# Performance work log

Hardware: AMD Instinct MI355X
Metric: run time of the kernel (lower is better)

The kernel has to match this reference:

```python
import jax, jax.numpy as jnp
import numpy as np

B, S, HID, NH, DH = 2, 1024, 4096, 32, 128
ACT_BITS, W_BITS = 8, 4
NEG_INF = float(np.finfo(np.float32).min)


def _qdq(x, bits):
    """Symmetric fake-quant over the last axis (per-token / per-out-channel), with STE."""
    qmax = 2.0 ** (bits - 1) - 1
    s = jnp.maximum(jnp.max(jnp.abs(x), axis=-1, keepdims=True) / qmax, 1e-8)
    q = jnp.clip(jnp.round(x / s), -qmax - 1, qmax) * s
    return x + jax.lax.stop_gradient(q - x)


def _rope_tables(seq_len, dim):
    inv_freq = 1.0 / (10000.0 ** (np.arange(0, dim, 2, dtype=np.float32) / dim))
    t = np.arange(seq_len, dtype=np.float32)
    freqs = np.outer(t, inv_freq)              # [S, DH/2]
    emb = np.concatenate([freqs, freqs], -1)   # [S, DH]
    return jnp.asarray(np.cos(emb)), jnp.asarray(np.sin(emb))


def _rotate_half(x):
    h = x.shape[-1] // 2
    return jnp.concatenate([-x[..., h:], x[..., :h]], axis=-1)


def _norm(x):
    return jnp.linalg.norm(x, axis=-1, keepdims=True)


def setup_inputs() -> dict:
    key = jax.random.key(0)
    ks = jax.random.split(key, 5)
    causal = jnp.where(jnp.tril(jnp.ones((S, S), dtype=bool)), 0.0, NEG_INF).astype(jnp.float32)
    return {
        "hidden_states": jax.random.normal(ks[0], (B, S, HID), jnp.float32),
        "wq": jax.random.normal(ks[1], (HID, HID), jnp.float32) * 0.02,
        "wk": jax.random.normal(ks[2], (HID, HID), jnp.float32) * 0.02,
        "wv": jax.random.normal(ks[3], (HID, HID), jnp.float32) * 0.02,
        "wo": jax.random.normal(ks[4], (HID, HID), jnp.float32) * 0.02,
        "attention_mask": jnp.broadcast_to(causal[None, None], (B, 1, S, S)),
    }


def reference(hidden_states, wq, wk, wv, wo, attention_mask):
    cos, sin = _rope_tables(S, DH)
    cos, sin = cos[None, None], sin[None, None]          # [1,1,S,DH]
    x = _qdq(hidden_states, ACT_BITS)                    # act fake-quant (per token)

    def proj(w):
        return jnp.einsum('bsh,dh->bsd', x, _qdq(w, W_BITS)).reshape(B, S, NH, DH).transpose(0, 2, 1, 3)

    q, k, v = proj(wq), proj(wk), proj(wv)               # [B,H,S,D]
    q = q * cos + _rotate_half(q) * sin
    k = k * cos + _rotate_half(k) * sin

    # qkt_matmul: quant Q and K, rescale scores by quantization norm ratios a1, a2
    x1len = _norm(q)
    qq = _qdq(q, ACT_BITS)
    a1 = _norm(qq) / x1len                               # [B,H,S,1]
    x2len = _norm(k)
    kq = _qdq(k, ACT_BITS)
    a2 = jnp.swapaxes(_norm(kq) / x2len, 2, 3)           # [B,H,1,S]

    attn = jnp.einsum('bhqd,bhkd->bhqk', qq, kq) / np.float32(np.sqrt(DH))
    attn = attn / a1 / a2
    attn = attn + attention_mask
    attn = jnp.maximum(attn, NEG_INF)
    p = jax.nn.softmax(attn.astype(jnp.float32), axis=-1)

    # pv_matmul: quant P and V, rescale output by V's norm ratio
    pq = _qdq(p, ACT_BITS)
    x2len_v = _norm(v)
    vq = _qdq(v, ACT_BITS)
    a2v = _norm(vq) / x2len_v                            # [B,H,S,1]

    out = jnp.einsum('bhqk,bhkd->bhqd', pq, vq) / a2v    # [B,H,S,D]
    out = out.transpose(0, 2, 1, 3).reshape(B, S, HID)
    out = jnp.einsum('bsh,dh->bsd', _qdq(out, ACT_BITS), _qdq(wo, W_BITS))
    return out
```

## Files before the change

kernel.cpp:

```cpp
#include <hip/hip_runtime.h>
#include <hip/hip_bf16.h>
#include <math.h>
#include <stdint.h>

#define NEG_INF_F (-3.4028234663852886e38f)

typedef __bf16 bf16_t;
typedef __bf16 bf16x8 __attribute__((ext_vector_type(8)));
typedef float f32x4 __attribute__((ext_vector_type(4)));
typedef float f32x16 __attribute__((ext_vector_type(16)));
typedef int i32x4 __attribute__((ext_vector_type(4)));
typedef int i32x16 __attribute__((ext_vector_type(16)));
typedef int8_t c8x4 __attribute__((ext_vector_type(4)));

static constexpr int Bb = 2, Ss = 1024, Hid = 4096, Nh = 32, Dh = 128;
static constexpr int Mr = Bb * Ss;
static constexpr int Bh = Bb * Nh;

__device__ __forceinline__ void gload_lds16(const void* g, void* l) {
  __builtin_amdgcn_global_load_lds((const __attribute__((address_space(1))) void*)g,
                                   (__attribute__((address_space(3))) void*)l, 16, 0, 0);
}

__device__ __forceinline__ float wred_max(float v) {
#pragma unroll
  for (int off = 32; off > 0; off >>= 1) v = fmaxf(v, __shfl_xor(v, off));
  return v;
}

__device__ __forceinline__ unsigned pkbf(float a, float b) {
  unsigned short ua = __builtin_bit_cast(unsigned short, (bf16_t)a);
  unsigned short ub = __builtin_bit_cast(unsigned short, (bf16_t)b);
  return (unsigned)ua | ((unsigned)ub << 16);
}

__global__ void rope_table_kernel(float* __restrict__ ctab, float* __restrict__ stab) {
  int i = blockIdx.x * 256 + threadIdx.x;
  int srow = i >> 6, d = i & 63;
  float invf = (float)pow(10000.0, -((double)(2 * d) / (double)Dh));
  float ang = (float)srow * invf;
  ctab[i] = (float)cos((double)ang);
  stab[i] = (float)sin((double)ang);
}

__global__ __launch_bounds__(256) void quant_rows_kernel(
    const float* __restrict__ in, int8_t* __restrict__ outq,
    float* __restrict__ scale, int ncols, float qmax, float clo, float chi)
{
  const int row = blockIdx.x;
  const float* x = in + (size_t)row * ncols;
  int8_t* o = outq + (size_t)row * ncols;
  const int tid = threadIdx.x;
  const float4* x4 = (const float4*)x;
  const int n4 = ncols >> 2;
  float m = 0.f;
  for (int i = tid; i < n4; i += 256) {
    float4 v = x4[i];
    m = fmaxf(m, fmaxf(fmaxf(fabsf(v.x), fabsf(v.y)), fmaxf(fabsf(v.z), fabsf(v.w))));
  }
  m = wred_max(m);
  __shared__ float red[4];
  if ((tid & 63) == 0) red[tid >> 6] = m;
  __syncthreads();
  m = fmaxf(fmaxf(red[0], red[1]), fmaxf(red[2], red[3]));
  const float s = fmaxf(m / qmax, 1e-8f);
  if (tid == 0) scale[row] = s;
  c8x4* o4 = (c8x4*)o;
  for (int i = tid; i < n4; i += 256) {
    float4 v = x4[i];
    c8x4 r;
    r[0] = (int8_t)(int)fminf(fmaxf(rintf(v.x / s), clo), chi);
    r[1] = (int8_t)(int)fminf(fmaxf(rintf(v.y / s), clo), chi);
    r[2] = (int8_t)(int)fminf(fmaxf(rintf(v.z / s), clo), chi);
    r[3] = (int8_t)(int)fminf(fmaxf(rintf(v.w / s), clo), chi);
    o4[i] = r;
  }
}

__global__ __launch_bounds__(256) void gemm_kernel(
    const int8_t* __restrict__ A, const float* __restrict__ sA,
    const int8_t* __restrict__ W, const float* __restrict__ sW,
    float* __restrict__ out, int M, int N, int K, int mode)
{
  __shared__ __align__(16) int8_t As[128 * 64];
  __shared__ __align__(16) int8_t Bs[128 * 64];
  const int tid = threadIdx.x, lane = tid & 63, wid = tid >> 6;
  const int bm = blockIdx.x * 128, bn = blockIdx.y * 128;
  const int wm = wid >> 1, wn = wid & 1;
  const int l15 = lane & 15, kg = lane >> 4;

  const int srow = wid * 16 + (lane >> 2);
  const int skin = (lane & 3) * 16;
  const int8_t* gA = A + (size_t)(bm + srow) * K + skin;
  const int8_t* gB = W + (size_t)(bn + srow) * K + skin;
  const size_t half = (size_t)64 * K;
  int8_t* lA = As + wid * 1024;
  int8_t* lB = Bs + wid * 1024;

  i32x4 acc[4][4] = {};
  for (int k0 = 0; k0 < K; k0 += 64) {
    if (k0) __syncthreads();
    gload_lds16(gA + k0, lA);
    gload_lds16(gA + k0 + half, lA + 4096);
    gload_lds16(gB + k0, lB);
    gload_lds16(gB + k0 + half, lB + 4096);
    __syncthreads();
    i32x4 af[4], bw[4];
#pragma unroll
    for (int f = 0; f < 4; ++f) {
      af[f] = *(const i32x4*)&As[(wm * 64 + f * 16 + l15) * 64 + kg * 16];
      bw[f] = *(const i32x4*)&Bs[(wn * 64 + f * 16 + l15) * 64 + kg * 16];
    }
#pragma unroll
    for (int fm = 0; fm < 4; ++fm)
#pragma unroll
      for (int fn = 0; fn < 4; ++fn)
        acc[fm][fn] = __builtin_amdgcn_mfma_i32_16x16x64_i8(af[fm], bw[fn], acc[fm][fn], 0, 0, 0);
  }
#pragma unroll
  for (int fm = 0; fm < 4; ++fm) {
    const int row0 = bm + wm * 64 + fm * 16 + kg * 4;
#pragma unroll
    for (int fn = 0; fn < 4; ++fn) {
      const int col = bn + wn * 64 + fn * 16 + l15;
      const float swv = sW[col];
#pragma unroll
      for (int j = 0; j < 4; ++j) {
        const int row = row0 + j;
        const float val = (float)acc[fm][fn][j] * sA[row] * swv;
        size_t off;
        if (mode == 0) off = (size_t)row * N + col;
        else {
          int b = row >> 10, si = row & 1023, h = col >> 7, d = col & 127;
          off = (((size_t)(b * Nh + h)) * Ss + si) * Dh + d;
        }
        out[off] = val;
      }
    }
  }
}

__global__ __launch_bounds__(256) void rope_quant_kernel(
    const float* __restrict__ xin,
    const float* __restrict__ ctab, const float* __restrict__ stab,
    int8_t* __restrict__ xq, float* __restrict__ F)
{
  const int gid = blockIdx.x * 4 + (threadIdx.x >> 6);
  const int lane = threadIdx.x & 63;
  const int srow = gid & (Ss - 1);
  const float* x = xin + (size_t)gid * Dh;
  const float xl = x[lane], xh = x[lane + 64];
  const float c = ctab[srow * 64 + lane], sn = stab[srow * 64 + lane];
  const float rl = __fsub_rn(__fmul_rn(xl, c), __fmul_rn(xh, sn));
  const float rh = __fadd_rn(__fmul_rn(xh, c), __fmul_rn(xl, sn));
  float ma = fmaxf(fabsf(rl), fabsf(rh));
  float n2 = rl * rl + rh * rh;
#pragma unroll
  for (int off = 32; off > 0; off >>= 1) {
    ma = fmaxf(ma, __shfl_xor(ma, off));
    n2 += __shfl_xor(n2, off);
  }
  const float s = fmaxf(ma / 127.0f, 1e-8f);
  const float ql = fminf(fmaxf(rintf(rl / s), -128.f), 127.f);
  const float qh = fminf(fmaxf(rintf(rh / s), -128.f), 127.f);
  float nq2 = ql * ql + qh * qh;
#pragma unroll
  for (int off = 32; off > 0; off >>= 1) nq2 += __shfl_xor(nq2, off);
  int8_t* o = xq + (size_t)gid * Dh;
  o[lane] = (int8_t)(int)ql;
  o[lane + 64] = (int8_t)(int)qh;
  if (lane == 0) F[gid] = sqrtf(n2 / nq2) * 0.2973017787506803f;
}

__global__ __launch_bounds__(256) void vquant_kernel(
    const float* __restrict__ vin, bf16_t* __restrict__ vdqt, float* __restrict__ a2v)
{
  __shared__ bf16_t s_v[128 * 66];
  const int tid = threadIdx.x, lane = tid & 63;
  const int l15 = lane & 15;
  const int qw = (tid >> 6) * 4 + (lane >> 4);
  const int bh = blockIdx.x >> 4;
  const int t0 = (blockIdx.x & 15) * 64;
  for (int it = 0; it < 4; ++it) {
    const int tt = qw * 4 + it;
    const size_t gid = (size_t)bh * Ss + t0 + tt;
    const float4 va = *(const float4*)(vin + gid * Dh + l15 * 8);
    const float4 vb = *(const float4*)(vin + gid * Dh + l15 * 8 + 4);
    float m = fmaxf(fmaxf(fmaxf(fabsf(va.x), fabsf(va.y)), fmaxf(fabsf(va.z), fabsf(va.w))),
                    fmaxf(fmaxf(fabsf(vb.x), fabsf(vb.y)), fmaxf(fabsf(vb.z), fabsf(vb.w))));
    float n2 = va.x * va.x + va.y * va.y + va.z * va.z + va.w * va.w +
               vb.x * vb.x + vb.y * vb.y + vb.z * vb.z + vb.w * vb.w;
#pragma unroll
    for (int off = 1; off < 16; off <<= 1) {
      m = fmaxf(m, __shfl_xor(m, off));
      n2 += __shfl_xor(n2, off);
    }
    const float s = fmaxf(m / 127.0f, 1e-8f);
    float q[8] = {va.x, va.y, va.z, va.w, vb.x, vb.y, vb.z, vb.w};
    float nq2 = 0.f;
#pragma unroll
    for (int e = 0; e < 8; ++e) {
      q[e] = fminf(fmaxf(rintf(q[e] / s), -128.f), 127.f);
      nq2 += q[e] * q[e];
      s_v[(l15 * 8 + e) * 66 + tt] = (bf16_t)(q[e] * s);
    }
#pragma unroll
    for (int off = 1; off < 16; off <<= 1) nq2 += __shfl_xor(nq2, off);
    if (l15 == 0) a2v[gid] = s * sqrtf(nq2) / sqrtf(n2);
  }
  __syncthreads();
  const int r = tid >> 1, hc = (tid & 1) * 32;
  const bf16_t* src = &s_v[r * 66 + hc];
  bf16_t* dst = vdqt + ((size_t)bh * Dh + r) * Ss + t0 + hc;
#pragma unroll
  for (int k = 0; k < 4; ++k) {
    bf16x8 t;
#pragma unroll
    for (int e = 0; e < 8; ++e) t[e] = src[k * 8 + e];
    *(bf16x8*)(dst + k * 8) = t;
  }
}

#define KR(r) (((r) & 3) + 8 * ((r) >> 2) + 4 * hi)
__global__ __launch_bounds__(64, 2) void attn_kernel(
    const int8_t* __restrict__ qq, const int8_t* __restrict__ kq,
    const bf16_t* __restrict__ vdqt,
    const float* __restrict__ Fq, const float* __restrict__ Fk,
    const float* __restrict__ A2v, float* __restrict__ oattn)
{
  const int bh = blockIdx.x, b = bh >> 5, h = bh & 31;
  const int lane = threadIdx.x & 63;
  const int l31 = lane & 31, hi = lane >> 5;
  const int u = 31 - (int)blockIdx.y;
  const int q0 = u * 32;
  const int nt = u + 1;
  const size_t bhS = (size_t)bh * Ss;

  const int8_t* qrow = qq + (bhS + q0 + l31) * Dh + hi * 16;
  i32x4 qf[4];
#pragma unroll
  for (int c = 0; c < 4; ++c) qf[c] = *(const i32x4*)(qrow + c * 32);
  const float fq = Fq[bhS + q0 + l31];
  const int qcol = q0 + l31;

  float m = NEG_INF_F;
  int t = 0;
  for (; t + 1 < nt; t += 2) {
    const int kb0 = t * 32, kb1 = kb0 + 32;
    const int8_t* kr0 = kq + (bhS + kb0 + l31) * Dh + hi * 16;
    const int8_t* kr1 = kq + (bhS + kb1 + l31) * Dh + hi * 16;
    i32x16 ca = {}, cb = {}, da = {}, db = {};
    ca = __builtin_amdgcn_mfma_i32_32x32x32_i8(*(const i32x4*)(kr0),      qf[0], ca, 0, 0, 0);
    cb = __builtin_amdgcn_mfma_i32_32x32x32_i8(*(const i32x4*)(kr0 + 64), qf[2], cb, 0, 0, 0);
    da = __builtin_amdgcn_mfma_i32_32x32x32_i8(*(const i32x4*)(kr1),      qf[0], da, 0, 0, 0);
    db = __builtin_amdgcn_mfma_i32_32x32x32_i8(*(const i32x4*)(kr1 + 64), qf[2], db, 0, 0, 0);
    ca = __builtin_amdgcn_mfma_i32_32x32x32_i8(*(const i32x4*)(kr0 + 32), qf[1], ca, 0, 0, 0);
    cb = __builtin_amdgcn_mfma_i32_32x32x32_i8(*(const i32x4*)(kr0 + 96), qf[3], cb, 0, 0, 0);
    da = __builtin_amdgcn_mfma_i32_32x32x32_i8(*(const i32x4*)(kr1 + 32), qf[1], da, 0, 0, 0);
    db = __builtin_amdgcn_mfma_i32_32x32x32_i8(*(const i32x4*)(kr1 + 96), qf[3], db, 0, 0, 0);
    float4 fk40[4], fk41[4];
#pragma unroll
    for (int g = 0; g < 4; ++g) fk40[g] = *(const float4*)&Fk[bhS + kb0 + g * 8 + 4 * hi];
#pragma unroll
    for (int g = 0; g < 4; ++g) fk41[g] = *(const float4*)&Fk[bhS + kb1 + g * 8 + 4 * hi];
    const bool diag1 = (t + 1 == nt - 1);
#pragma unroll
    for (int r = 0; r < 16; ++r) {
      m = fmaxf(m, (float)(ca[r] + cb[r]) * fq * ((const float*)&fk40[r >> 2])[r & 3]);
      const float v1 = (float)(da[r] + db[r]) * fq * ((const float*)&fk41[r >> 2])[r & 3];
      if (!diag1 || (kb1 + KR(r) <= qcol)) m = fmaxf(m, v1);
    }
  }
  if (t < nt) {
    const int kb = t * 32;
    const int8_t* krow = kq + (bhS + kb + l31) * Dh + hi * 16;
    i32x16 ca = {}, cb = {};
    ca = __builtin_amdgcn_mfma_i32_32x32x32_i8(*(const i32x4*)(krow),      qf[0], ca, 0, 0, 0);
    cb = __builtin_amdgcn_mfma_i32_32x32x32_i8(*(const i32x4*)(krow + 64), qf[2], cb, 0, 0, 0);
    ca = __builtin_amdgcn_mfma_i32_32x32x32_i8(*(const i32x4*)(krow + 32), qf[1], ca, 0, 0, 0);
    cb = __builtin_amdgcn_mfma_i32_32x32x32_i8(*(const i32x4*)(krow + 96), qf[3], cb, 0, 0, 0);
    float4 fk4[4];
#pragma unroll
    for (int g = 0; g < 4; ++g) fk4[g] = *(const float4*)&Fk[bhS + kb + g * 8 + 4 * hi];
#pragma unroll
    for (int r = 0; r < 16; ++r) {
      const float v = (float)(ca[r] + cb[r]) * fq * ((const float*)&fk4[r >> 2])[r & 3];
      if (kb + KR(r) <= qcol) m = fmaxf(m, v);
    }
  }
  m = fmaxf(m, __shfl_xor(m, 32));

  float z = 0.f;
  f32x16 oacc[4] = {};
  for (int tt = 0; tt < nt; ++tt) {
    const int kb = tt * 32;
    const int8_t* krow = kq + (bhS + kb + l31) * Dh + hi * 16;
    i32x16 ca = {}, cb = {};
    ca = __builtin_amdgcn_mfma_i32_32x32x32_i8(*(const i32x4*)(krow),      qf[0], ca, 0, 0, 0);
    cb = __builtin_amdgcn_mfma_i32_32x32x32_i8(*(const i32x4*)(krow + 64), qf[2], cb, 0, 0, 0);
    ca = __builtin_amdgcn_mfma_i32_32x32x32_i8(*(const i32x4*)(krow + 32), qf[1], ca, 0, 0, 0);
    cb = __builtin_amdgcn_mfma_i32_32x32x32_i8(*(const i32x4*)(krow + 96), qf[3], cb, 0, 0, 0);
    float4 fk4[4];
#pragma unroll
    for (int g = 0; g < 4; ++g) fk4[g] = *(const float4*)&Fk[bhS + kb + g * 8 + 4 * hi];
    float p[16];
    const bool diag = (tt == nt - 1);
#pragma unroll
    for (int r = 0; r < 16; ++r) {
      float v = (float)(ca[r] + cb[r]) * fq * ((const float*)&fk4[r >> 2])[r & 3];
      if (diag && (kb + KR(r) > qcol)) v = NEG_INF_F;
      const float e = __expf(v - m);
      z += e;
      p[r] = rintf(127.0f * e);
    }
#pragma unroll
    for (int s = 0; s < 2; ++s) {
      const int rs = s * 8;
      unsigned k0 = pkbf(p[rs + 0], p[rs + 1]);
      unsigned k1 = pkbf(p[rs + 2], p[rs + 3]);
      unsigned k2 = pkbf(p[rs + 4], p[rs + 5]);
      unsigned k3 = pkbf(p[rs + 6], p[rs + 7]);
      unsigned sx0 = __shfl_xor(k0, 32);
      unsigned sx1 = __shfl_xor(k1, 32);
      unsigned sx2 = __shfl_xor(k2, 32);
      unsigned sx3 = __shfl_xor(k3, 32);
      uint4 ww;
      ww.x = hi ? sx2 : k0;
      ww.y = hi ? sx3 : k1;
      ww.z = hi ? k2 : sx0;
      ww.w = hi ? k3 : sx1;
      const bf16x8 af = __builtin_bit_cast(bf16x8, ww);
      const int kg = kb + s * 16 + hi * 8;
#pragma unroll
      for (int dt = 0; dt < 4; ++dt) {
        const bf16x8 vf = *(const bf16x8*)(vdqt + ((size_t)bh * Dh + dt * 32 + l31) * Ss + kg);
        oacc[dt] = __builtin_amdgcn_mfma_f32_32x32x16_bf16(af, vf, oacc[dt], 0, 0, 0);
      }
    }
  }
  z += __shfl_xor(z, 32);
  const float osc = (1.0f / z) / 127.0f / A2v[bhS + q0 + l31];
#pragma unroll
  for (int dt = 0; dt < 4; ++dt) {
#pragma unroll
    for (int r = 0; r < 16; ++r) {
      const int q = q0 + KR(r);
      const float oscr = __shfl(osc, KR(r));
      oattn[((size_t)b * Ss + q) * Hid + h * Dh + dt * 32 + l31] = oacc[dt][r] * oscr;
    }
  }
}

extern "C" void kernel_launch(void* const* d_in, const int* in_sizes, int n_in,
                              void* d_out, int out_size, void* d_ws, size_t ws_size,
                              hipStream_t stream)
{
  const float* hidden = (const float*)d_in[0];
  const float* wq = (const float*)d_in[1];
  const float* wk = (const float*)d_in[2];
  const float* wv = (const float*)d_in[3];
  const float* wo = (const float*)d_in[4];
  float* out = (float*)d_out;

  char* p = (char*)d_ws;
  auto alloc = [&](size_t bytes) -> char* {
    char* r = p; p += (bytes + 255) & ~(size_t)255; return r;
  };
  int8_t* xq   = (int8_t*)alloc((size_t)Mr * Hid);
  int8_t* wbuf = (int8_t*)alloc((size_t)Hid * Hid);
  float*  projf= (float*) alloc((size_t)Bh * Ss * Dh * sizeof(float));
  int8_t* qqb  = (int8_t*)alloc((size_t)Bh * Ss * Dh);
  int8_t* kqb  = (int8_t*)alloc((size_t)Bh * Ss * Dh);
  bf16_t* vdqt = (bf16_t*)alloc((size_t)Bh * Dh * Ss * sizeof(bf16_t));
  float* sxa = (float*)alloc((size_t)Mr * sizeof(float));
  float* sw  = (float*)alloc((size_t)Hid * sizeof(float));
  float* Fq  = (float*)alloc((size_t)Bh * Ss * sizeof(float));
  float* Fk  = (float*)alloc((size_t)Bh * Ss * sizeof(float));
  float* A2v = (float*)alloc((size_t)Bh * Ss * sizeof(float));
  float* soa = (float*)alloc((size_t)Mr * sizeof(float));
  float* ctab = (float*)alloc((size_t)Ss * 64 * sizeof(float));
  float* stab = (float*)alloc((size_t)Ss * 64 * sizeof(float));
  float*  oat = projf;
  int8_t* oq  = xq;

  rope_table_kernel<<<Ss * 64 / 256, 256, 0, stream>>>(ctab, stab);
  quant_rows_kernel<<<Mr, 256, 0, stream>>>(hidden, xq, sxa, Hid, 127.f, -128.f, 127.f);

  dim3 gg(Mr / 128, Hid / 128);
  quant_rows_kernel<<<Hid, 256, 0, stream>>>(wq, wbuf, sw, Hid, 7.f, -8.f, 7.f);
  gemm_kernel<<<gg, 256, 0, stream>>>(xq, sxa, wbuf, sw, projf, Mr, Hid, Hid, 1);
  rope_quant_kernel<<<Bh * Ss / 4, 256, 0, stream>>>(projf, ctab, stab, qqb, Fq);
  quant_rows_kernel<<<Hid, 256, 0, stream>>>(wk, wbuf, sw, Hid, 7.f, -8.f, 7.f);
  gemm_kernel<<<gg, 256, 0, stream>>>(xq, sxa, wbuf, sw, projf, Mr, Hid, Hid, 1);
  rope_quant_kernel<<<Bh * Ss / 4, 256, 0, stream>>>(projf, ctab, stab, kqb, Fk);
  quant_rows_kernel<<<Hid, 256, 0, stream>>>(wv, wbuf, sw, Hid, 7.f, -8.f, 7.f);
  gemm_kernel<<<gg, 256, 0, stream>>>(xq, sxa, wbuf, sw, projf, Mr, Hid, Hid, 1);
  vquant_kernel<<<Bh * 16, 256, 0, stream>>>(projf, vdqt, A2v);

  dim3 ga(Bh, 32);
  attn_kernel<<<ga, 64, 0, stream>>>(qqb, kqb, vdqt, Fq, Fk, A2v, oat);

  quant_rows_kernel<<<Mr, 256, 0, stream>>>(oat, oq, soa, Hid, 127.f, -128.f, 127.f);
  quant_rows_kernel<<<Hid, 256, 0, stream>>>(wo, wbuf, sw, Hid, 7.f, -8.f, 7.f);
  gemm_kernel<<<gg, 256, 0, stream>>>(oq, soa, wbuf, sw, out, Mr, Hid, Hid, 0);
}
```

Measured before the change: 446.9 us.

## Fuse RoPE and per-head quantization into QKV GEMM epilogues, swizzle LDS and blocks

Q/K projection GEMMs now apply RoPE, per-token-per-head int8 quantization and the norm-ratio factor directly in the epilogue. The V GEMM quantizes, transposes through shared memory and writes bf16 V^T plus A2v. This removes the fp32 projection round-trip and the separate rope_quant and vquant kernels. Column fragments are remapped so each 128-wide N tile holds one head with matching rotate-half pairs in registers. The change also adds an XOR swizzle on the LDS k-chunks and an XCD-aware block ordering, at the cost of more registers and extra epilogue syncs.

```diff
diff --git a/kernel.cpp b/kernel.cpp
--- a/kernel.cpp
+++ b/kernel.cpp
@@ -77,22 +77,36 @@
   }
 }
 
+template <int MODE>
 __global__ __launch_bounds__(256) void gemm_kernel(
     const int8_t* __restrict__ A, const float* __restrict__ sA,
     const int8_t* __restrict__ W, const float* __restrict__ sW,
-    float* __restrict__ out, int M, int N, int K, int mode)
+    float* __restrict__ out0,
+    int8_t* __restrict__ outq, float* __restrict__ Ff,
+    bf16_t* __restrict__ vdq, float* __restrict__ a2vp,
+    const float* __restrict__ ctab, const float* __restrict__ stab,
+    int M, int N, int K)
 {
   __shared__ __align__(16) int8_t As[128 * 64];
   __shared__ __align__(16) int8_t Bs[128 * 64];
+  __shared__ float s_red[2][128][3];
+  __shared__ __align__(16) char smem_vt[MODE == 3 ? (128 * 136 * 2) : 16];
+
   const int tid = threadIdx.x, lane = tid & 63, wid = tid >> 6;
-  const int bm = blockIdx.x * 128, bn = blockIdx.y * 128;
+  const int id = blockIdx.x;
+  const int xcd = id & 7, within = id >> 3;
+  const int nIdx = xcd * 4 + (within >> 4);
+  const int mIdx = within & 15;
+  const int bm = mIdx * 128, bn = nIdx * 128;
+
   const int wm = wid >> 1, wn = wid & 1;
   const int l15 = lane & 15, kg = lane >> 4;
-
-  const int srow = wid * 16 + (lane >> 2);
-  const int skin = (lane & 3) * 16;
-  const int8_t* gA = A + (size_t)(bm + srow) * K + skin;
-  const int8_t* gB = W + (size_t)(bn + srow) * K + skin;
+  const int ckey = (l15 >> 1) & 3;
+
+  const int srowL = wid * 16 + (lane >> 2);
+  const int skin = ((lane & 3) ^ ((lane >> 3) & 3)) * 16;
+  const int8_t* gA = A + (size_t)(bm + srowL) * K + skin;
+  const int8_t* gB = W + (size_t)(bn + srowL) * K + skin;
   const size_t half = (size_t)64 * K;
   int8_t* lA = As + wid * 1024;
   int8_t* lB = Bs + wid * 1024;
@@ -108,8 +122,8 @@
     i32x4 af[4], bw[4];
 #pragma unroll
     for (int f = 0; f < 4; ++f) {
-      af[f] = *(const i32x4*)&As[(wm * 64 + f * 16 + l15) * 64 + kg * 16];
-      bw[f] = *(const i32x4*)&Bs[(wn * 64 + f * 16 + l15) * 64 + kg * 16];
+      af[f] = *(const i32x4*)&As[(wm * 64 + f * 16 + l15) * 64 + (kg ^ ckey) * 16];
+      bw[f] = *(const i32x4*)&Bs[(f * 32 + wn * 16 + l15) * 64 + (kg ^ ckey) * 16];
     }
 #pragma unroll
     for (int fm = 0; fm < 4; ++fm)
@@ -117,107 +131,169 @@
       for (int fn = 0; fn < 4; ++fn)
         acc[fm][fn] = __builtin_amdgcn_mfma_i32_16x16x64_i8(af[fm], bw[fn], acc[fm][fn], 0, 0, 0);
   }
-#pragma unroll
-  for (int fm = 0; fm < 4; ++fm) {
-    const int row0 = bm + wm * 64 + fm * 16 + kg * 4;
-#pragma unroll
-    for (int fn = 0; fn < 4; ++fn) {
-      const int col = bn + wn * 64 + fn * 16 + l15;
-      const float swv = sW[col];
+
+  float sav[4][4], swv[4];
+#pragma unroll
+  for (int fm = 0; fm < 4; ++fm)
+#pragma unroll
+    for (int j = 0; j < 4; ++j) sav[fm][j] = sA[bm + wm * 64 + fm * 16 + kg * 4 + j];
+#pragma unroll
+  for (int fn = 0; fn < 4; ++fn) swv[fn] = sW[bn + fn * 32 + wn * 16 + l15];
+
+  float val[4][4][4];
+#pragma unroll
+  for (int fm = 0; fm < 4; ++fm)
+#pragma unroll
+    for (int fn = 0; fn < 4; ++fn)
+#pragma unroll
+      for (int j = 0; j < 4; ++j)
+        val[fm][fn][j] = (float)acc[fm][fn][j] * sav[fm][j] * swv[fn];
+
+  if constexpr (MODE == 0) {
+#pragma unroll
+    for (int fm = 0; fm < 4; ++fm)
 #pragma unroll
       for (int j = 0; j < 4; ++j) {
-        const int row = row0 + j;
-        const float val = (float)acc[fm][fn][j] * sA[row] * swv;
-        size_t off;
-        if (mode == 0) off = (size_t)row * N + col;
-        else {
-          int b = row >> 10, si = row & 1023, h = col >> 7, d = col & 127;
-          off = (((size_t)(b * Nh + h)) * Ss + si) * Dh + d;
-        }
-        out[off] = val;
+        const int row = bm + wm * 64 + fm * 16 + kg * 4 + j;
+#pragma unroll
+        for (int fn = 0; fn < 4; ++fn)
+          out0[(size_t)row * N + bn + fn * 32 + wn * 16 + l15] = val[fm][fn][j];
       }
-    }
-  }
-}
-
-__global__ __launch_bounds__(256) void rope_quant_kernel(
-    const float* __restrict__ xin,
-    const float* __restrict__ ctab, const float* __restrict__ stab,
-    int8_t* __restrict__ xq, float* __restrict__ F)
-{
-  const int gid = blockIdx.x * 4 + (threadIdx.x >> 6);
-  const int lane = threadIdx.x & 63;
-  const int srow = gid & (Ss - 1);
-  const float* x = xin + (size_t)gid * Dh;
-  const float xl = x[lane], xh = x[lane + 64];
-  const float c = ctab[srow * 64 + lane], sn = stab[srow * 64 + lane];
-  const float rl = __fsub_rn(__fmul_rn(xl, c), __fmul_rn(xh, sn));
-  const float rh = __fadd_rn(__fmul_rn(xh, c), __fmul_rn(xl, sn));
-  float ma = fmaxf(fabsf(rl), fabsf(rh));
-  float n2 = rl * rl + rh * rh;
-#pragma unroll
-  for (int off = 32; off > 0; off >>= 1) {
-    ma = fmaxf(ma, __shfl_xor(ma, off));
-    n2 += __shfl_xor(n2, off);
-  }
-  const float s = fmaxf(ma / 127.0f, 1e-8f);
-  const float ql = fminf(fmaxf(rintf(rl / s), -128.f), 127.f);
-  const float qh = fminf(fmaxf(rintf(rh / s), -128.f), 127.f);
-  float nq2 = ql * ql + qh * qh;
-#pragma unroll
-  for (int off = 32; off > 0; off >>= 1) nq2 += __shfl_xor(nq2, off);
-  int8_t* o = xq + (size_t)gid * Dh;
-  o[lane] = (int8_t)(int)ql;
-  o[lane + 64] = (int8_t)(int)qh;
-  if (lane == 0) F[gid] = sqrtf(n2 / nq2) * 0.2973017787506803f;
-}
-
-__global__ __launch_bounds__(256) void vquant_kernel(
-    const float* __restrict__ vin, bf16_t* __restrict__ vdqt, float* __restrict__ a2v)
-{
-  __shared__ bf16_t s_v[128 * 66];
-  const int tid = threadIdx.x, lane = tid & 63;
-  const int l15 = lane & 15;
-  const int qw = (tid >> 6) * 4 + (lane >> 4);
-  const int bh = blockIdx.x >> 4;
-  const int t0 = (blockIdx.x & 15) * 64;
-  for (int it = 0; it < 4; ++it) {
-    const int tt = qw * 4 + it;
-    const size_t gid = (size_t)bh * Ss + t0 + tt;
-    const float4 va = *(const float4*)(vin + gid * Dh + l15 * 8);
-    const float4 vb = *(const float4*)(vin + gid * Dh + l15 * 8 + 4);
-    float m = fmaxf(fmaxf(fmaxf(fabsf(va.x), fabsf(va.y)), fmaxf(fabsf(va.z), fabsf(va.w))),
-                    fmaxf(fmaxf(fabsf(vb.x), fabsf(vb.y)), fmaxf(fabsf(vb.z), fabsf(vb.w))));
-    float n2 = va.x * va.x + va.y * va.y + va.z * va.z + va.w * va.w +
-               vb.x * vb.x + vb.y * vb.y + vb.z * vb.z + vb.w * vb.w;
-#pragma unroll
-    for (int off = 1; off < 16; off <<= 1) {
-      m = fmaxf(m, __shfl_xor(m, off));
-      n2 += __shfl_xor(n2, off);
-    }
-    const float s = fmaxf(m / 127.0f, 1e-8f);
-    float q[8] = {va.x, va.y, va.z, va.w, vb.x, vb.y, vb.z, vb.w};
-    float nq2 = 0.f;
-#pragma unroll
-    for (int e = 0; e < 8; ++e) {
-      q[e] = fminf(fmaxf(rintf(q[e] / s), -128.f), 127.f);
-      nq2 += q[e] * q[e];
-      s_v[(l15 * 8 + e) * 66 + tt] = (bf16_t)(q[e] * s);
-    }
-#pragma unroll
-    for (int off = 1; off < 16; off <<= 1) nq2 += __shfl_xor(nq2, off);
-    if (l15 == 0) a2v[gid] = s * sqrtf(nq2) / sqrtf(n2);
-  }
-  __syncthreads();
-  const int r = tid >> 1, hc = (tid & 1) * 32;
-  const bf16_t* src = &s_v[r * 66 + hc];
-  bf16_t* dst = vdqt + ((size_t)bh * Dh + r) * Ss + t0 + hc;
-#pragma unroll
-  for (int k = 0; k < 4; ++k) {
-    bf16x8 t;
-#pragma unroll
-    for (int e = 0; e < 8; ++e) t[e] = src[k * 8 + e];
-    *(bf16x8*)(dst + k * 8) = t;
+  } else {
+    const int b = bm >> 10;
+    const int bh = b * Nh + nIdx;
+    float r_[4][4][4];
+    if constexpr (MODE == 2) {
+      const int dmA = wn * 16 + l15, dmB = 32 + wn * 16 + l15;
+#pragma unroll
+      for (int fm = 0; fm < 4; ++fm)
+#pragma unroll
+        for (int j = 0; j < 4; ++j) {
+          const int srow = (bm + wm * 64 + fm * 16 + kg * 4 + j) & (Ss - 1);
+          const float cA = ctab[srow * 64 + dmA], cB = ctab[srow * 64 + dmB];
+          const float sA_ = stab[srow * 64 + dmA], sB_ = stab[srow * 64 + dmB];
+          r_[fm][0][j] = __fsub_rn(__fmul_rn(val[fm][0][j], cA), __fmul_rn(val[fm][2][j], sA_));
+          r_[fm][1][j] = __fsub_rn(__fmul_rn(val[fm][1][j], cB), __fmul_rn(val[fm][3][j], sB_));
+          r_[fm][2][j] = __fadd_rn(__fmul_rn(val[fm][2][j], cA), __fmul_rn(val[fm][0][j], sA_));
+          r_[fm][3][j] = __fadd_rn(__fmul_rn(val[fm][3][j], cB), __fmul_rn(val[fm][1][j], sB_));
+        }
+    } else {
+#pragma unroll
+      for (int fm = 0; fm < 4; ++fm)
+#pragma unroll
+        for (int fn = 0; fn < 4; ++fn)
+#pragma unroll
+          for (int j = 0; j < 4; ++j) r_[fm][fn][j] = val[fm][fn][j];
+    }
+    float ma_[4][4], n2_[4][4];
+#pragma unroll
+    for (int fm = 0; fm < 4; ++fm)
+#pragma unroll
+      for (int j = 0; j < 4; ++j) {
+        float ma = 0.f, n2 = 0.f;
+#pragma unroll
+        for (int fn = 0; fn < 4; ++fn) {
+          const float x = r_[fm][fn][j];
+          ma = fmaxf(ma, fabsf(x));
+          n2 += x * x;
+        }
+#pragma unroll
+        for (int off = 1; off < 16; off <<= 1) {
+          ma = fmaxf(ma, __shfl_xor(ma, off));
+          n2 += __shfl_xor(n2, off);
+        }
+        ma_[fm][j] = ma;
+        n2_[fm][j] = n2;
+      }
+    if (l15 == 0) {
+#pragma unroll
+      for (int fm = 0; fm < 4; ++fm)
+#pragma unroll
+        for (int j = 0; j < 4; ++j) {
+          const int rl = wm * 64 + fm * 16 + kg * 4 + j;
+          s_red[wn][rl][0] = ma_[fm][j];
+          s_red[wn][rl][1] = n2_[fm][j];
+        }
+    }
+    __syncthreads();
+    float qc[4][4][4], svl[4][4], n2c[4][4], nq2_[4][4];
+#pragma unroll
+    for (int fm = 0; fm < 4; ++fm)
+#pragma unroll
+      for (int j = 0; j < 4; ++j) {
+        const int rl = wm * 64 + fm * 16 + kg * 4 + j;
+        const float ma = fmaxf(ma_[fm][j], s_red[wn ^ 1][rl][0]);
+        const float n2 = n2_[fm][j] + s_red[wn ^ 1][rl][1];
+        const float s = fmaxf(ma / 127.0f, 1e-8f);
+        float nq2 = 0.f;
+#pragma unroll
+        for (int fn = 0; fn < 4; ++fn) {
+          const float q = fminf(fmaxf(rintf(r_[fm][fn][j] / s), -128.f), 127.f);
+          qc[fm][fn][j] = q;
+          nq2 += q * q;
+        }
+#pragma unroll
+        for (int off = 1; off < 16; off <<= 1) nq2 += __shfl_xor(nq2, off);
+        svl[fm][j] = s;
+        n2c[fm][j] = n2;
+        nq2_[fm][j] = nq2;
+      }
+    if (l15 == 0) {
+#pragma unroll
+      for (int fm = 0; fm < 4; ++fm)
+#pragma unroll
+        for (int j = 0; j < 4; ++j)
+          s_red[wn][wm * 64 + fm * 16 + kg * 4 + j][2] = nq2_[fm][j];
+    }
+    __syncthreads();
+
+    if constexpr (MODE == 2) {
+#pragma unroll
+      for (int fm = 0; fm < 4; ++fm)
+#pragma unroll
+        for (int j = 0; j < 4; ++j) {
+          const int rl = wm * 64 + fm * 16 + kg * 4 + j;
+          const int stok = (bm + rl) & (Ss - 1);
+          const size_t rowBase = ((size_t)bh * Ss + stok) * Dh;
+#pragma unroll
+          for (int fn = 0; fn < 4; ++fn)
+            outq[rowBase + fn * 32 + wn * 16 + l15] = (int8_t)(int)qc[fm][fn][j];
+          if (wn == 0 && l15 == 0) {
+            const float nq2 = nq2_[fm][j] + s_red[1][rl][2];
+            Ff[(size_t)bh * Ss + stok] = sqrtf(n2c[fm][j] / nq2) * 0.2973017787506803f;
+          }
+        }
+    } else {
+      bf16_t* svt = (bf16_t*)smem_vt;
+#pragma unroll
+      for (int fm = 0; fm < 4; ++fm)
+#pragma unroll
+        for (int j = 0; j < 4; ++j) {
+          const int t = wm * 64 + fm * 16 + kg * 4 + j;
+#pragma unroll
+          for (int fn = 0; fn < 4; ++fn) {
+            const int d = fn * 32 + wn * 16 + l15;
+            svt[d * 136 + t] = (bf16_t)(qc[fm][fn][j] * svl[fm][j]);
+          }
+          if (wn == 0 && l15 == 0) {
+            const float nq2 = nq2_[fm][j] + s_red[1][t][2];
+            a2vp[(size_t)bh * Ss + ((bm + t) & (Ss - 1))] =
+                svl[fm][j] * sqrtf(nq2) / sqrtf(n2c[fm][j]);
+          }
+        }
+      __syncthreads();
+      const int d = tid >> 1, toff = (tid & 1) * 64;
+      const int s0 = bm & (Ss - 1);
+      const bf16_t* src = svt + d * 136 + toff;
+      bf16_t* dst = vdq + ((size_t)bh * Dh + d) * Ss + s0 + toff;
+#pragma unroll
+      for (int k = 0; k < 8; ++k) {
+        bf16x8 tv;
+#pragma unroll
+        for (int e = 0; e < 8; ++e) tv[e] = src[k * 8 + e];
+        *(bf16x8*)(dst + k * 8) = tv;
+      }
+    }
   }
 }
 
@@ -330,10 +406,10 @@
       ww.z = hi ? k2 : sx0;
       ww.w = hi ? k3 : sx1;
       const bf16x8 af = __builtin_bit_cast(bf16x8, ww);
-      const int kg = kb + s * 16 + hi * 8;
+      const int kg2 = kb + s * 16 + hi * 8;
 #pragma unroll
       for (int dt = 0; dt < 4; ++dt) {
-        const bf16x8 vf = *(const bf16x8*)(vdqt + ((size_t)bh * Dh + dt * 32 + l31) * Ss + kg);
+        const bf16x8 vf = *(const bf16x8*)(vdqt + ((size_t)bh * Dh + dt * 32 + l31) * Ss + kg2);
         oacc[dt] = __builtin_amdgcn_mfma_f32_32x32x16_bf16(af, vf, oacc[dt], 0, 0, 0);
       }
     }
@@ -368,7 +444,7 @@
   };
   int8_t* xq   = (int8_t*)alloc((size_t)Mr * Hid);
   int8_t* wbuf = (int8_t*)alloc((size_t)Hid * Hid);
-  float*  projf= (float*) alloc((size_t)Bh * Ss * Dh * sizeof(float));
+  float*  oat  = (float*) alloc((size_t)Bh * Ss * Dh * sizeof(float));
   int8_t* qqb  = (int8_t*)alloc((size_t)Bh * Ss * Dh);
   int8_t* kqb  = (int8_t*)alloc((size_t)Bh * Ss * Dh);
   bf16_t* vdqt = (bf16_t*)alloc((size_t)Bh * Dh * Ss * sizeof(bf16_t));
@@ -380,27 +456,26 @@
   float* soa = (float*)alloc((size_t)Mr * sizeof(float));
   float* ctab = (float*)alloc((size_t)Ss * 64 * sizeof(float));
   float* stab = (float*)alloc((size_t)Ss * 64 * sizeof(float));
-  float*  oat = projf;
   int8_t* oq  = xq;
 
   rope_table_kernel<<<Ss * 64 / 256, 256, 0, stream>>>(ctab, stab);
   quant_rows_kernel<<<Mr, 256, 0, stream>>>(hidden, xq, sxa, Hid, 127.f, -128.f, 127.f);
 
-  dim3 gg(Mr / 128, Hid / 128);
   quant_rows_kernel<<<Hid, 256, 0, stream>>>(wq, wbuf, sw, Hid, 7.f, -8.f, 7.f);
-  gemm_kernel<<<gg, 256, 0, stream>>>(xq, sxa, wbuf, sw, projf, Mr, Hid, Hid, 1);
-  rope_quant_kernel<<<Bh * Ss / 4, 256, 0, stream>>>(projf, ctab, stab, qqb, Fq);
+  gemm_kernel<2><<<512, 256, 0, stream>>>(xq, sxa, wbuf, sw, nullptr, qqb, Fq,
+                                          nullptr, nullptr, ctab, stab, Mr, Hid, Hid);
   quant_rows_kernel<<<Hid, 256, 0, stream>>>(wk, wbuf, sw, Hid, 7.f, -8.f, 7.f);
-  gemm_kernel<<<gg, 256, 0, stream>>>(xq, sxa, wbuf, sw, projf, Mr, Hid, Hid, 1);
-  rope_quant_kernel<<<Bh * Ss / 4, 256, 0, stream>>>(projf, ctab, stab, kqb, Fk);
+  gemm_kernel<2><<<512, 256, 0, stream>>>(xq, sxa, wbuf, sw, nullptr, kqb, Fk,
+                                          nullptr, nullptr, ctab, stab, Mr, Hid, Hid);
   quant_rows_kernel<<<Hid, 256, 0, stream>>>(wv, wbuf, sw, Hid, 7.f, -8.f, 7.f);
-  gemm_kernel<<<gg, 256, 0, stream>>>(xq, sxa, wbuf, sw, projf, Mr, Hid, Hid, 1);
-  vquant_kernel<<<Bh * 16, 256, 0, stream>>>(projf, vdqt, A2v);
+  gemm_kernel<3><<<512, 256, 0, stream>>>(xq, sxa, wbuf, sw, nullptr, nullptr, nullptr,
+                                          vdqt, A2v, ctab, stab, Mr, Hid, Hid);
 
   dim3 ga(Bh, 32);
   attn_kernel<<<ga, 64, 0, stream>>>(qqb, kqb, vdqt, Fq, Fk, A2v, oat);
 
   quant_rows_kernel<<<Mr, 256, 0, stream>>>(oat, oq, soa, Hid, 127.f, -128.f, 127.f);
   quant_rows_kernel<<<Hid, 256, 0, stream>>>(wo, wbuf, sw, Hid, 7.f, -8.f, 7.f);
-  gemm_kernel<<<gg, 256, 0, stream>>>(oq, soa, wbuf, sw, out, Mr, Hid, Hid, 0);
-}
+  gemm_kernel<0><<<512, 256, 0, stream>>>(oq, soa, wbuf, sw, out, nullptr, nullptr,
+                                          nullptr, nullptr, nullptr, nullptr, Mr, Hid, Hid);
+}
```

Measured after the change: 411.2 us. -8.0%, faster.
